# Kernel optimization log

Hardware: AMD Instinct MI355X
Metric: run time of the kernel (lower is better)

## Reference

```python
import jax, jax.numpy as jnp
import numpy as np

WIN = 9
EPS = 1e-05


def _box3d(x, win=WIN):
    """Sum over a win^3 box (zero-padded), equivalent to conv3d with a ones kernel.
    Implemented as three separable 1D convolutions (exact same math, O(win)/voxel)."""
    pad = win // 2
    for axis in range(3):  # spatial axes D, H, W
        kshape = [1, 1, 1, 1, 1]
        kshape[2 + axis] = win
        kern = jnp.ones(kshape, x.dtype)
        pads = [(0, 0)] * 3
        pads[axis] = (pad, pad)
        dn = jax.lax.conv_dimension_numbers(x.shape, kern.shape, ('NCDHW', 'OIDHW', 'NCDHW'))
        x = jax.lax.conv_general_dilated(x, kern, window_strides=(1, 1, 1),
                                         padding=pads, dimension_numbers=dn)
    return x


def setup_inputs() -> dict:
    key = jax.random.key(0)
    k1, k2 = jax.random.split(key)
    shape = (1, 1, 160, 192, 224)  # [N, C, D, H, W] brain-MRI-scale volume
    I = jax.random.normal(k1, shape, dtype=jnp.float32)
    J = jax.random.normal(k2, shape, dtype=jnp.float32)
    return {"I": I, "J": J}


def reference(I, J):
    win_size = WIN ** 3
    I2 = I * I
    J2 = J * J
    IJ = I * J
    I_sum = _box3d(I)
    J_sum = _box3d(J)
    I2_sum = _box3d(I2)
    J2_sum = _box3d(J2)
    IJ_sum = _box3d(IJ)
    u_I = I_sum / win_size
    u_J = J_sum / win_size
    cross = IJ_sum - u_J * I_sum - u_I * J_sum + u_I * u_J * win_size
    I_var = I2_sum - 2 * u_I * I_sum + u_I * u_I * win_size
    J_var = J2_sum - 2 * u_J * J_sum + u_J * u_J * win_size
    cc = cross * cross / (I_var * J_var + EPS)
    return -1.0 * jnp.mean(cc)
```

## Files before the change

kernel.cpp:

```cpp
#include <hip/hip_runtime.h>


#define DD 160
#define HH 192
#define WW 224
#define W4 56
#define SLICE (HH * WW)
#define S4 (SLICE / 4)
#define NVOX (DD * SLICE)
#define TW 32
#define TH 8
#define DCH 28
#define ITERS (DCH + 8)
#define NTHR 256
#define SW_RS 36
#define SW_CS (16 * SW_RS)
#define SH_SZ (TH * TW * 5)
#define EPS 1e-5f
#define INV_WSUM (1.0f / 729.0f)

__device__ __forceinline__ void bar_lds_only() {
    __asm__ volatile("" ::: "memory");
    __builtin_amdgcn_s_waitcnt(0xC07F);
    __builtin_amdgcn_s_barrier();
    __asm__ volatile("" ::: "memory");
}

__global__ __launch_bounds__(NTHR, 4) void ncc_fused(const float* __restrict__ I,
                                                     const float* __restrict__ J,
                                                     float* __restrict__ out) {
    __shared__ float SW0[5 * SW_CS], SW1[5 * SW_CS];
    __shared__ float SH0[SH_SZ], SH1[SH_SZ];
    __shared__ float wred[NTHR / 64];

    const int tid = threadIdx.x;
    const int tx = tid & 31, ty = tid >> 5;
    const int wlo = blockIdx.x * TW;
    const int hlo = blockIdx.y * TH;
    const int dlo = blockIdx.z * DCH;

    const int wid = tid - 128;
    const int wr = wid >> 3, wc = wid & 7;
    const int gh = hlo - 4 + wr;
    const bool hok = (gh >= 0) && (gh < HH);
    const int gf0 = (wlo >> 2) - 1 + wc;

    const int hcol = tid & 31, hch = tid >> 5;

    const float4* Iv = (const float4*)I;
    const float4* Jv = (const float4*)J;

    float pfa[12], pfb[12];

    auto w_load = [&](int z) {
        const bool zok = (z >= 0) && (z < DD) && hok;
        const int rowb = z * S4 + gh * W4;
        #pragma unroll
        for (int k = 0; k < 3; ++k) {
            const int f = gf0 + k;
            float4 a = make_float4(0.f, 0.f, 0.f, 0.f);
            float4 b = make_float4(0.f, 0.f, 0.f, 0.f);
            if (zok && f >= 0 && f < W4) { a = Iv[rowb + f]; b = Jv[rowb + f]; }
            pfa[4*k] = a.x; pfa[4*k+1] = a.y; pfa[4*k+2] = a.z; pfa[4*k+3] = a.w;
            pfb[4*k] = b.x; pfb[4*k+1] = b.y; pfb[4*k+2] = b.z; pfb[4*k+3] = b.w;
        }
    };

    auto w_compute = [&](float* dst) {
        float* wp = dst + wr * SW_RS + 4 * wc;
        #pragma unroll
        for (int ch = 0; ch < 5; ++ch) {
            float v[12];
            #pragma unroll
            for (int k = 0; k < 12; ++k)
                v[k] = (ch == 0) ? pfa[k]
                     : (ch == 1) ? pfb[k]
                     : (ch == 2) ? pfa[k] * pfa[k]
                     : (ch == 3) ? pfb[k] * pfb[k]
                     :             pfa[k] * pfb[k];
            float s = v[0];
            #pragma unroll
            for (int k = 1; k < 9; ++k) s += v[k];
            float4 o;
            o.x = s;
            s += v[9]  - v[0]; o.y = s;
            s += v[10] - v[1]; o.z = s;
            s += v[11] - v[2]; o.w = s;
            *(float4*)(wp + ch * SW_CS) = o;
        }
    };

    auto h_phase = [&](const float* swSrc, float* shDst) {
        const float* p = swSrc + hch * SW_CS + hcol;
        float v[16];
        #pragma unroll
        for (int r = 0; r < 16; r += 2) {
            const float* pr = p + r * SW_RS;
            v[r]     = pr[0];
            v[r + 1] = pr[SW_RS];
        }
        float s = v[0];
        #pragma unroll
        for (int r = 1; r < 9; ++r) s += v[r];
        float* o = shDst + hcol * 5 + hch;
        float prev = s;
        o[0] = s;
        #pragma unroll
        for (int r = 1; r < TH; ++r) {
            prev += v[r + 8] - v[r - 1];
            o[r * (TW * 5)] = prev;
        }
    };

    float q0[9], q1[9], q2[9], q3[9], q4[9];
    #pragma unroll
    for (int k = 0; k < 9; ++k) { q0[k]=0.f; q1[k]=0.f; q2[k]=0.f; q3[k]=0.f; q4[k]=0.f; }
    float r0=0.f, r1=0.f, r2=0.f, r3=0.f, r4=0.f;
    float acc = 0.f;

    const int z0 = dlo - 4;
    if (tid >= 128) {
        w_load(z0);
        if (z0 >= 0) w_compute(SW0);
        w_load(z0 + 1);
    }
    bar_lds_only();

    if (tid < 160 && z0 >= 0) h_phase(SW0, SH0);
    if (tid >= 128) {
        const int z1 = z0 + 1;
        if (z1 >= 0 && z1 < DD) w_compute(SW1);
        w_load(z0 + 2);
    }

    #pragma unroll 1
    for (int g = 0; g < 4; ++g) {
        #pragma unroll
        for (int ph = 0; ph < 9; ++ph) {
            const int j = 9 * g + ph;
            const int z = dlo - 4 + j;
            bar_lds_only();

            const bool val = (z >= 0) && (z < DD);
            float* shR = (j & 1) ? SH1 : SH0;
            float w0=0.f, w1=0.f, w2=0.f, w3=0.f, w4=0.f;
            if (val) {
                const float* pF = shR + (ty * TW + tx) * 5;
                w0 = pF[0]; w1 = pF[1]; w2 = pF[2]; w3 = pF[3]; w4 = pF[4];
            }

            if ((g < 3 || ph < 8) && tid < 160) {
                const int zh = z + 1;
                if (zh >= 0 && zh < DD)
                    h_phase((j & 1) ? SW0 : SW1, (j & 1) ? SH0 : SH1);
            }

            if ((g < 3 || ph < 7) && tid >= 128) {
                const int zw = z + 2;
                if (zw >= 0 && zw < DD) w_compute((j & 1) ? SW1 : SW0);
                w_load(z + 3);
            }

            r0 += w0 - q0[ph]; q0[ph] = w0;
            r1 += w1 - q1[ph]; q1[ph] = w1;
            r2 += w2 - q2[ph]; q2[ph] = w2;
            r3 += w3 - q3[ph]; q3[ph] = w3;
            r4 += w4 - q4[ph]; q4[ph] = w4;

            if (j >= 8 && (dlo + j - 8) < DD) {
                float cross = r4 - r0 * r1 * INV_WSUM;
                float iv    = r2 - r0 * r0 * INV_WSUM;
                float jv    = r3 - r1 * r1 * INV_WSUM;
                acc += cross * cross * __builtin_amdgcn_rcpf(iv * jv + EPS);
            }
        }
    }

    #pragma unroll
    for (int off = 32; off > 0; off >>= 1) acc += __shfl_down(acc, off, 64);
    if ((tid & 63) == 0) wred[tid >> 6] = acc;
    __syncthreads();
    if (tid == 0) {
        float t = 0.f;
        #pragma unroll
        for (int k = 0; k < NTHR / 64; ++k) t += wred[k];
        atomicAdd(out, t * (-1.0f / (float)NVOX));
    }
}

extern "C" void kernel_launch(void* const* d_in, const int* in_sizes, int n_in,
                              void* d_out, int out_size, void* d_ws, size_t ws_size,
                              hipStream_t stream) {
    const float* I = (const float*)d_in[0];
    const float* J = (const float*)d_in[1];
    float* out = (float*)d_out;

    hipMemsetAsync(d_out, 0, sizeof(float), stream);

    dim3 blk(NTHR, 1, 1);
    dim3 grd(WW / TW, HH / TH, (DD + DCH - 1) / DCH);
    ncc_fused<<<grd, blk, 0, stream>>>(I, J, out);
}
```

Baseline: 126.0 us.

## Replace H-pass staging buffers with in-place prefix sums and triple-buffered W slices

Drops the separate SH staging buffers. The H pass now writes an in-place prefix sum along H into a triple-buffered W-sum slice, and the consumer reads each 9-row box sum as the difference of two prefix entries. The warp roles are swapped: waves 0-1 now load and do the W pass, and waves 2-3 do the H prefix pass. This cuts LDS traffic and the footprint of the transposed stores, at the cost of a third LDS slice buffer and a float prefix-sum difference that may lose some precision.

```diff
diff --git a/kernel.cpp b/kernel.cpp
--- a/kernel.cpp
+++ b/kernel.cpp
@@ -14,8 +14,7 @@
 #define ITERS (DCH + 8)
 #define NTHR 256
 #define SW_RS 36
-#define SW_CS (16 * SW_RS)
-#define SH_SZ (TH * TW * 5)
+#define SW_CS (17 * SW_RS)
 #define EPS 1e-5f
 #define INV_WSUM (1.0f / 729.0f)
 
@@ -29,8 +28,7 @@
 __global__ __launch_bounds__(NTHR, 4) void ncc_fused(const float* __restrict__ I,
                                                      const float* __restrict__ J,
                                                      float* __restrict__ out) {
-    __shared__ float SW0[5 * SW_CS], SW1[5 * SW_CS];
-    __shared__ float SH0[SH_SZ], SH1[SH_SZ];
+    __shared__ float SW0[5 * SW_CS], SW1[5 * SW_CS], SW2[5 * SW_CS];
     __shared__ float wred[NTHR / 64];
 
     const int tid = threadIdx.x;
@@ -39,13 +37,13 @@
     const int hlo = blockIdx.y * TH;
     const int dlo = blockIdx.z * DCH;
 
-    const int wid = tid - 128;
-    const int wr = wid >> 3, wc = wid & 7;
+    const int wr = tid >> 3, wc = tid & 7;
     const int gh = hlo - 4 + wr;
     const bool hok = (gh >= 0) && (gh < HH);
     const int gf0 = (wlo >> 2) - 1 + wc;
 
-    const int hcol = tid & 31, hch = tid >> 5;
+    const int ht = tid - 128;
+    const int hcol = ht & 31, hch = ht >> 5;
 
     const float4* Iv = (const float4*)I;
     const float4* Jv = (const float4*)J;
@@ -67,7 +65,7 @@
     };
 
     auto w_compute = [&](float* dst) {
-        float* wp = dst + wr * SW_RS + 4 * wc;
+        float* wp = dst + (wr + 1) * SW_RS + 4 * wc;
         #pragma unroll
         for (int ch = 0; ch < 5; ++ch) {
             float v[12];
@@ -90,26 +88,31 @@
         }
     };
 
-    auto h_phase = [&](const float* swSrc, float* shDst) {
-        const float* p = swSrc + hch * SW_CS + hcol;
+    auto h_one = [&](float* buf, int col, int ch) {
+        float* base = buf + ch * SW_CS + col;
         float v[16];
         #pragma unroll
         for (int r = 0; r < 16; r += 2) {
-            const float* pr = p + r * SW_RS;
+            const float* pr = base + (r + 1) * SW_RS;
             v[r]     = pr[0];
             v[r + 1] = pr[SW_RS];
         }
-        float s = v[0];
-        #pragma unroll
-        for (int r = 1; r < 9; ++r) s += v[r];
-        float* o = shDst + hcol * 5 + hch;
-        float prev = s;
-        o[0] = s;
-        #pragma unroll
-        for (int r = 1; r < TH; ++r) {
-            prev += v[r + 8] - v[r - 1];
-            o[r * (TW * 5)] = prev;
-        }
+        base[0] = 0.f;
+        float run = 0.f;
+        #pragma unroll
+        for (int r = 0; r < 16; ++r) {
+            run += v[r];
+            base[(r + 1) * SW_RS] = run;
+        }
+    };
+
+    auto h_phase = [&](float* buf) {
+        h_one(buf, hcol, hch);
+        if (ht < 32) h_one(buf, hcol, 4);
+    };
+
+    auto bsel = [&](int m) -> float* {
+        return (m == 0) ? SW0 : (m == 1) ? SW1 : SW2;
     };
 
     float q0[9], q1[9], q2[9], q3[9], q4[9];
@@ -119,15 +122,14 @@
     float acc = 0.f;
 
     const int z0 = dlo - 4;
-    if (tid >= 128) {
+    if (tid < 128) {
         w_load(z0);
         if (z0 >= 0) w_compute(SW0);
         w_load(z0 + 1);
     }
     bar_lds_only();
-
-    if (tid < 160 && z0 >= 0) h_phase(SW0, SH0);
-    if (tid >= 128) {
+    if (tid >= 128 && z0 >= 0) h_phase(SW0);
+    if (tid < 128) {
         const int z1 = z0 + 1;
         if (z1 >= 0 && z1 < DD) w_compute(SW1);
         w_load(z0 + 2);
@@ -142,22 +144,24 @@
             bar_lds_only();
 
             const bool val = (z >= 0) && (z < DD);
-            float* shR = (j & 1) ? SH1 : SH0;
             float w0=0.f, w1=0.f, w2=0.f, w3=0.f, w4=0.f;
             if (val) {
-                const float* pF = shR + (ty * TW + tx) * 5;
-                w0 = pF[0]; w1 = pF[1]; w2 = pF[2]; w3 = pF[3]; w4 = pF[4];
-            }
-
-            if ((g < 3 || ph < 8) && tid < 160) {
+                const float* pb = bsel(ph % 3) + ty * SW_RS + tx;
+                w0 = pb[9*SW_RS]              - pb[0];
+                w1 = pb[SW_CS   + 9*SW_RS]    - pb[SW_CS];
+                w2 = pb[2*SW_CS + 9*SW_RS]    - pb[2*SW_CS];
+                w3 = pb[3*SW_CS + 9*SW_RS]    - pb[3*SW_CS];
+                w4 = pb[4*SW_CS + 9*SW_RS]    - pb[4*SW_CS];
+            }
+
+            if (j < ITERS - 1 && tid >= 128) {
                 const int zh = z + 1;
-                if (zh >= 0 && zh < DD)
-                    h_phase((j & 1) ? SW0 : SW1, (j & 1) ? SH0 : SH1);
-            }
-
-            if ((g < 3 || ph < 7) && tid >= 128) {
+                if (zh >= 0 && zh < DD) h_phase(bsel((ph + 1) % 3));
+            }
+
+            if (j < ITERS - 2 && tid < 128) {
                 const int zw = z + 2;
-                if (zw >= 0 && zw < DD) w_compute((j & 1) ? SW1 : SW0);
+                if (zw >= 0 && zw < DD) w_compute(bsel((ph + 2) % 3));
                 w_load(z + 3);
             }
 
```

New measurement: 131.7 us. 4.4% more time.

## Fuse W and H box passes using DPP lane shifts, drop intermediate LDS stage

Applied to the files above, without the earlier changes.

Replaces the separate W-sum (LDS write) and H-sum (LDS read/write) phases with a single phase. Every thread loads a row segment and computes the 9-wide W sums, then does the 9-tall H sum across lanes with DPP row_shr adds (a shift-and-add tree), writing only the final 2D sums to LDS. All 256 threads now take part instead of split producer groups. This removes one LDS round trip and shortens the pipeline by one stage, and it moves the barrier to the end of each step. The cost is duplicated loads (each lane pair covers 2 channel sets) and DPP tree adds whose validity depends on the row layout (16-lane rows).

```diff
diff --git a/kernel.cpp b/kernel.cpp
--- a/kernel.cpp
+++ b/kernel.cpp
@@ -13,9 +13,9 @@
 #define DCH 28
 #define ITERS (DCH + 8)
 #define NTHR 256
-#define SW_RS 36
-#define SW_CS (16 * SW_RS)
-#define SH_SZ (TH * TW * 5)
+#define SH_RS 36
+#define SH_CS 292
+#define SH_SZ (5 * SH_CS)
 #define EPS 1e-5f
 #define INV_WSUM (1.0f / 729.0f)
 
@@ -26,26 +26,43 @@
     __asm__ volatile("" ::: "memory");
 }
 
+template <int N>
+__device__ __forceinline__ float sr_add(float acc, float x) {
+    int sh = __builtin_amdgcn_update_dpp(0, __float_as_int(x),
+                                         0x110 | N, 0xF, 0xF, true);
+    return acc + __int_as_float(sh);
+}
+
+__device__ __forceinline__ float vert9(float v) {
+    float s1 = sr_add<1>(v, v);
+    float s2 = sr_add<2>(s1, s1);
+    float s4 = sr_add<4>(s2, s2);
+    return sr_add<8>(s4, v);
+}
+
 __global__ __launch_bounds__(NTHR, 4) void ncc_fused(const float* __restrict__ I,
                                                      const float* __restrict__ J,
                                                      float* __restrict__ out) {
-    __shared__ float SW0[5 * SW_CS], SW1[5 * SW_CS];
     __shared__ float SH0[SH_SZ], SH1[SH_SZ];
     __shared__ float wred[NTHR / 64];
 
     const int tid = threadIdx.x;
-    const int tx = tid & 31, ty = tid >> 5;
     const int wlo = blockIdx.x * TW;
     const int hlo = blockIdx.y * TH;
     const int dlo = blockIdx.z * DCH;
 
-    const int wid = tid - 128;
-    const int wr = wid >> 3, wc = wid & 7;
-    const int gh = hlo - 4 + wr;
+    const int lane = tid & 63;
+    const int wv   = tid >> 6;
+    const int sub  = lane >> 5;
+    const int r16  = lane & 15;
+    const int g    = 2 * wv + ((lane >> 4) & 1);
+    const int gh   = hlo - 4 + r16;
     const bool hok = (gh >= 0) && (gh < HH);
-    const int gf0 = (wlo >> 2) - 1 + wc;
+    const int gf0  = (wlo >> 2) - 1 + g;
+    const bool wrt = ((lane >> 3) & 1) != 0;
+    const int crow = lane & 7;
 
-    const int hcol = tid & 31, hch = tid >> 5;
+    const int fx = tid & 31, fy = tid >> 5;
 
     const float4* Iv = (const float4*)I;
     const float4* Jv = (const float4*)J;
@@ -66,18 +83,16 @@
         }
     };
 
-    auto w_compute = [&](float* dst) {
-        float* wp = dst + wr * SW_RS + 4 * wc;
+    auto wh_phase = [&](float* shDst) {
         #pragma unroll
-        for (int ch = 0; ch < 5; ++ch) {
+        for (int t = 0; t < 3; ++t) {
+            if (t == 2 && sub) continue;
             float v[12];
             #pragma unroll
             for (int k = 0; k < 12; ++k)
-                v[k] = (ch == 0) ? pfa[k]
-                     : (ch == 1) ? pfb[k]
-                     : (ch == 2) ? pfa[k] * pfa[k]
-                     : (ch == 3) ? pfb[k] * pfb[k]
-                     :             pfa[k] * pfb[k];
+                v[k] = (t == 0) ? (sub ? pfb[k] * pfb[k] : pfa[k])
+                     : (t == 1) ? (sub ? pfa[k] * pfb[k] : pfb[k])
+                     :            pfa[k] * pfa[k];
             float s = v[0];
             #pragma unroll
             for (int k = 1; k < 9; ++k) s += v[k];
@@ -86,29 +101,13 @@
             s += v[9]  - v[0]; o.y = s;
             s += v[10] - v[1]; o.z = s;
             s += v[11] - v[2]; o.w = s;
-            *(float4*)(wp + ch * SW_CS) = o;
-        }
-    };
-
-    auto h_phase = [&](const float* swSrc, float* shDst) {
-        const float* p = swSrc + hch * SW_CS + hcol;
-        float v[16];
-        #pragma unroll
-        for (int r = 0; r < 16; r += 2) {
-            const float* pr = p + r * SW_RS;
-            v[r]     = pr[0];
-            v[r + 1] = pr[SW_RS];
-        }
-        float s = v[0];
-        #pragma unroll
-        for (int r = 1; r < 9; ++r) s += v[r];
-        float* o = shDst + hcol * 5 + hch;
-        float prev = s;
-        o[0] = s;
-        #pragma unroll
-        for (int r = 1; r < TH; ++r) {
-            prev += v[r + 8] - v[r - 1];
-            o[r * (TW * 5)] = prev;
+            float4 sv;
+            sv.x = vert9(o.x); sv.y = vert9(o.y);
+            sv.z = vert9(o.z); sv.w = vert9(o.w);
+            if (wrt) {
+                const int ch = sub ? (3 + t) : t;
+                *(float4*)(shDst + ch * SH_CS + crow * SH_RS + 4 * g) = sv;
+            }
         }
     };
 
@@ -119,46 +118,35 @@
     float acc = 0.f;
 
     const int z0 = dlo - 4;
-    if (tid >= 128) {
-        w_load(z0);
-        if (z0 >= 0) w_compute(SW0);
-        w_load(z0 + 1);
-    }
+    w_load(z0);
+    if (z0 >= 0) wh_phase(SH0);
+    w_load(z0 + 1);
     bar_lds_only();
 
-    if (tid < 160 && z0 >= 0) h_phase(SW0, SH0);
-    if (tid >= 128) {
-        const int z1 = z0 + 1;
-        if (z1 >= 0 && z1 < DD) w_compute(SW1);
-        w_load(z0 + 2);
-    }
-
     #pragma unroll 1
-    for (int g = 0; g < 4; ++g) {
+    for (int gg = 0; gg < 4; ++gg) {
         #pragma unroll
         for (int ph = 0; ph < 9; ++ph) {
-            const int j = 9 * g + ph;
+            const int j = 9 * gg + ph;
             const int z = dlo - 4 + j;
-            bar_lds_only();
-
             const bool val = (z >= 0) && (z < DD);
             float* shR = (j & 1) ? SH1 : SH0;
+            float* shW = (j & 1) ? SH0 : SH1;
+
             float w0=0.f, w1=0.f, w2=0.f, w3=0.f, w4=0.f;
             if (val) {
-                const float* pF = shR + (ty * TW + tx) * 5;
-                w0 = pF[0]; w1 = pF[1]; w2 = pF[2]; w3 = pF[3]; w4 = pF[4];
+                const float* pF = shR + fy * SH_RS + fx;
+                w0 = pF[0];
+                w1 = pF[SH_CS];
+                w2 = pF[2 * SH_CS];
+                w3 = pF[3 * SH_CS];
+                w4 = pF[4 * SH_CS];
             }
 
-            if ((g < 3 || ph < 8) && tid < 160) {
+            if (j < ITERS - 1) {
                 const int zh = z + 1;
-                if (zh >= 0 && zh < DD)
-                    h_phase((j & 1) ? SW0 : SW1, (j & 1) ? SH0 : SH1);
-            }
-
-            if ((g < 3 || ph < 7) && tid >= 128) {
-                const int zw = z + 2;
-                if (zw >= 0 && zw < DD) w_compute((j & 1) ? SW1 : SW0);
-                w_load(z + 3);
+                if (zh >= 0 && zh < DD) wh_phase(shW);
+                w_load(z + 2);
             }
 
             r0 += w0 - q0[ph]; q0[ph] = w0;
@@ -173,6 +161,7 @@
                 float jv    = r3 - r1 * r1 * INV_WSUM;
                 acc += cross * cross * __builtin_amdgcn_rcpf(iv * jv + EPS);
             }
+            bar_lds_only();
         }
     }
 
```

After: 173.5 us. 1.38x slower.

## Balance W-phase and H-phase work evenly across all four wavefronts

Applied to the files above, without the earlier changes.

Previously only waves 2-3 did the global loads and W-direction box sums, and waves 0-2 did the H-phase, so the per-wave load was uneven. Now both 128-thread halves load the same I/J data, with one half computing the I, J and I² channels and the other computing J² and IJ. The 160 H-phase tasks are spread as 40 lanes in each of the four waves. This shortens the critical wave's work per slice, but every voxel row is now loaded twice from global memory and part of each wave sits idle in the H-phase.

```diff
diff --git a/kernel.cpp b/kernel.cpp
--- a/kernel.cpp
+++ b/kernel.cpp
@@ -39,13 +39,17 @@
     const int hlo = blockIdx.y * TH;
     const int dlo = blockIdx.z * DCH;
 
-    const int wid = tid - 128;
-    const int wr = wid >> 3, wc = wid & 7;
+    const int half = tid >> 7;
+    const int rg   = tid & 127;
+    const int wr = rg >> 3, wc = rg & 7;
     const int gh = hlo - 4 + wr;
     const bool hok = (gh >= 0) && (gh < HH);
     const int gf0 = (wlo >> 2) - 1 + wc;
 
-    const int hcol = tid & 31, hch = tid >> 5;
+    const int lane = tid & 63;
+    const int htask = (tid >> 6) * 40 + lane;
+    const bool hact = lane < 40;
+    const int hcol = htask & 31, hch = htask >> 5;
 
     const float4* Iv = (const float4*)I;
     const float4* Jv = (const float4*)J;
@@ -69,15 +73,15 @@
     auto w_compute = [&](float* dst) {
         float* wp = dst + wr * SW_RS + 4 * wc;
         #pragma unroll
-        for (int ch = 0; ch < 5; ++ch) {
+        for (int t = 0; t < 3; ++t) {
+            if (half && t == 2) break;
             float v[12];
             #pragma unroll
             for (int k = 0; k < 12; ++k)
-                v[k] = (ch == 0) ? pfa[k]
-                     : (ch == 1) ? pfb[k]
-                     : (ch == 2) ? pfa[k] * pfa[k]
-                     : (ch == 3) ? pfb[k] * pfb[k]
-                     :             pfa[k] * pfb[k];
+                v[k] = half ? ((t == 0) ? pfb[k] * pfb[k] : pfa[k] * pfb[k])
+                            : ((t == 0) ? pfa[k]
+                             : (t == 1) ? pfb[k]
+                             :            pfa[k] * pfa[k]);
             float s = v[0];
             #pragma unroll
             for (int k = 1; k < 9; ++k) s += v[k];
@@ -86,6 +90,7 @@
             s += v[9]  - v[0]; o.y = s;
             s += v[10] - v[1]; o.z = s;
             s += v[11] - v[2]; o.w = s;
+            const int ch = half ? (3 + t) : t;
             *(float4*)(wp + ch * SW_CS) = o;
         }
     };
@@ -119,15 +124,13 @@
     float acc = 0.f;
 
     const int z0 = dlo - 4;
-    if (tid >= 128) {
-        w_load(z0);
-        if (z0 >= 0) w_compute(SW0);
-        w_load(z0 + 1);
-    }
+    w_load(z0);
+    if (z0 >= 0) w_compute(SW0);
+    w_load(z0 + 1);
     bar_lds_only();
 
-    if (tid < 160 && z0 >= 0) h_phase(SW0, SH0);
-    if (tid >= 128) {
+    if (hact && z0 >= 0) h_phase(SW0, SH0);
+    {
         const int z1 = z0 + 1;
         if (z1 >= 0 && z1 < DD) w_compute(SW1);
         w_load(z0 + 2);
@@ -149,13 +152,13 @@
                 w0 = pF[0]; w1 = pF[1]; w2 = pF[2]; w3 = pF[3]; w4 = pF[4];
             }
 
-            if ((g < 3 || ph < 8) && tid < 160) {
+            if ((g < 3 || ph < 8) && hact) {
                 const int zh = z + 1;
                 if (zh >= 0 && zh < DD)
                     h_phase((j & 1) ? SW0 : SW1, (j & 1) ? SH0 : SH1);
             }
 
-            if ((g < 3 || ph < 7) && tid >= 128) {
+            if (g < 3 || ph < 7) {
                 const int zw = z + 2;
                 if (zw >= 0 && zw < DD) w_compute((j & 1) ? SW1 : SW0);
                 w_load(z + 3);
```

Measured after the change: 130.0 us. 3.2% more time.
